# Optimization experiments

Measured on AMD Instinct MI355X. Metric: run time of the kernel, lower is better.

## Reference

```python
import jax, jax.numpy as jnp
import numpy as np

NUM_HEADS = 20


def _rope(t, pos):
    """Rotary embedding (ESM style, rotate_half on full head_dim).
    t: (T, h, d), pos: (T,) float32 position within each sequence."""
    d = t.shape[-1]
    inv_freq = 1.0 / (10000.0 ** (jnp.arange(0, d, 2, dtype=jnp.float32) / d))  # (d/2,)
    freqs = pos[:, None] * inv_freq[None, :]          # (T, d/2)
    emb = jnp.concatenate([freqs, freqs], axis=-1)    # (T, d)
    cos = jnp.cos(emb)[:, None, :]                    # (T, 1, d)
    sin = jnp.sin(emb)[:, None, :]
    x1, x2 = jnp.split(t, 2, axis=-1)
    rot = jnp.concatenate([-x2, x1], axis=-1)
    return t * cos + rot * sin


def setup_inputs() -> dict:
    key = jax.random.key(0)
    ks = jax.random.split(key, 8)
    E = 1280
    lengths = np.array([512, 768, 1024, 1024, 1024, 1280, 1280, 1280], dtype=np.int64)
    cu_lens = jnp.asarray(np.concatenate([[0], np.cumsum(lengths)]).astype(np.int32))
    T = int(lengths.sum())  # 8192
    s = (2.0 / (E + E)) ** 0.5  # xavier-ish scale
    return {
        "x": jax.random.normal(ks[0], (T, E), jnp.float32),
        "cu_lens": cu_lens,
        "max_len": 1280,
        "Wq": jax.random.normal(ks[1], (E, E), jnp.float32) * s,
        "bq": jnp.zeros((E,), jnp.float32),
        "Wk": jax.random.normal(ks[2], (E, E), jnp.float32) * s,
        "bk": jnp.zeros((E,), jnp.float32),
        "Wv": jax.random.normal(ks[3], (E, E), jnp.float32) * s,
        "bv": jnp.zeros((E,), jnp.float32),
        "Wo": jax.random.normal(ks[4], (E, E), jnp.float32) * (2.0 ** 0.5) * s,
        "bo": jnp.zeros((E,), jnp.float32),
    }


def reference(x, cu_lens, max_len, Wq, bq, Wk, bk, Wv, bv, Wo, bo):
    T, E = x.shape
    h = NUM_HEADS
    d = E // h
    scale = d ** -0.5
    # fused QKV projections (q pre-scaled, softmax_scale=1 as in the original)
    q = ((x @ Wq.T + bq) * scale).reshape(T, h, d)
    k = (x @ Wk.T + bk).reshape(T, h, d)
    v = (x @ Wv.T + bv).reshape(T, h, d)
    # per-token sequence id and within-sequence position from cu_lens
    t_idx = jnp.arange(T)
    seq_id = jnp.searchsorted(cu_lens, t_idx, side='right') - 1  # (T,)
    pos = t_idx - cu_lens[seq_id]                                # (T,) int
    # rotary on q and k with per-sequence positions
    posf = pos.astype(jnp.float32)
    q = _rope(q, posf)
    k = _rope(k, posf)
    # scatter packed tokens into padded (B, max_len, h, d) layout
    B = cu_lens.shape[0] - 1
    qp = jnp.zeros((B, max_len, h, d), q.dtype).at[seq_id, pos].set(q)
    kp = jnp.zeros((B, max_len, h, d), k.dtype).at[seq_id, pos].set(k)
    vp = jnp.zeros((B, max_len, h, d), v.dtype).at[seq_id, pos].set(v)
    valid = jnp.zeros((B, max_len), bool).at[seq_id, pos].set(True)
    # non-causal attention within each sequence (block-diagonal over packed tokens)
    scores = jnp.einsum('blhd,bmhd->bhlm', qp, kp)
    scores = jnp.where(valid[:, None, None, :], scores, -1e9)
    attn = jax.nn.softmax(scores, axis=-1)
    o = jnp.einsum('bhlm,bmhd->blhd', attn, vp)
    # gather back to packed layout and apply output projection
    out_tok = o[seq_id, pos].reshape(T, E)
    return out_tok @ Wo.T + bo
```

## Files before the change

kernel.cpp:

```cpp
#include <hip/hip_runtime.h>
#include <hip/hip_bf16.h>
#include <cstdint>

#define E_DIM   1280
#define NHEADS  20
#define HDIM    64
#define QKV_LD  3840

typedef __attribute__((ext_vector_type(8))) short bf8_t;
typedef __attribute__((ext_vector_type(4))) short bf4_t;
typedef __attribute__((ext_vector_type(4))) float f4_t;

__device__ __forceinline__ short f2bs(float f) {
    union { __hip_bfloat16 h; short s; } u;
    u.h = __float2bfloat16(f);
    return u.s;
}

__device__ __forceinline__ bf4_t pk4(f4_t s) {
    union { bf4_t v; uint32_t u[2]; } r;
    asm("v_cvt_pk_bf16_f32 %0, %1, %2" : "=v"(r.u[0]) : "v"(s[0]), "v"(s[1]));
    asm("v_cvt_pk_bf16_f32 %0, %1, %2" : "=v"(r.u[1]) : "v"(s[2]), "v"(s[3]));
    return r.v;
}

__device__ __forceinline__ f4_t mfma16x32(bf8_t a, bf8_t b, f4_t c) {
    return __builtin_amdgcn_mfma_f32_16x16x32_bf16(a, b, c, 0, 0, 0);
}
__device__ __forceinline__ f4_t mfma16x16(bf4_t a, bf4_t b, f4_t c) {
    return __builtin_amdgcn_mfma_f32_16x16x16bf16_1k(a, b, c, 0, 0, 0);
}

__device__ __forceinline__ void gl_lds16(const void* g, void* l) {
    auto gp = reinterpret_cast<__attribute__((address_space(1))) unsigned int*>(
        reinterpret_cast<uintptr_t>(g));
    auto lp = reinterpret_cast<__attribute__((address_space(3))) unsigned int*>(
        reinterpret_cast<uintptr_t>(l));
    __builtin_amdgcn_global_load_lds(gp, lp, 16, 0, 0);
}

#define QSCALE 0.18033688011112042f

__device__ __forceinline__ void cvt8(__hip_bfloat16* dst, const float* src, float sc) {
    float4 a = *(const float4*)src;
    float4 b = *(const float4*)(src + 4);
    bf8_t v;
    v[0] = f2bs(a.x * sc); v[1] = f2bs(a.y * sc); v[2] = f2bs(a.z * sc); v[3] = f2bs(a.w * sc);
    v[4] = f2bs(b.x * sc); v[5] = f2bs(b.y * sc); v[6] = f2bs(b.z * sc); v[7] = f2bs(b.w * sc);
    *(bf8_t*)dst = v;
}

__global__ __launch_bounds__(256) void prep_kernel(
    const float* __restrict__ x,
    const float* __restrict__ wq, const float* __restrict__ wk,
    const float* __restrict__ wv, const float* __restrict__ wo,
    const float* __restrict__ bq, const float* __restrict__ bk, const float* __restrict__ bv,
    __hip_bfloat16* __restrict__ xbf, __hip_bfloat16* __restrict__ wqkv,
    __hip_bfloat16* __restrict__ wobf, float* __restrict__ bqkv,
    long nx8, long nw8, long nb8)
{
    long u = (long)blockIdx.x * 256 + threadIdx.x;
    if (u < nx8) { cvt8(xbf + u * 8, x + u * 8, 1.0f); return; }
    u -= nx8;
    if (u < 3 * nw8) {
        long e = u * 8;
        long w1 = nw8 * 8;
        const float* src; float sc;
        if (e < w1)            { src = wq + e;           sc = QSCALE; }
        else if (e < 2 * w1)   { src = wk + (e - w1);    sc = 1.0f; }
        else                   { src = wv + (e - 2*w1);  sc = 1.0f; }
        cvt8(wqkv + e, src, sc);
        return;
    }
    u -= 3 * nw8;
    if (u < nw8) { cvt8(wobf + u * 8, wo + u * 8, 1.0f); return; }
    u -= nw8;
    if (u < nb8) {
        long e = u * 8;
        #pragma unroll
        for (int j = 0; j < 8; j++) {
            long i = e + j;
            float v;
            if (i < E_DIM)           v = bq[i] * QSCALE;
            else if (i < 2 * E_DIM)  v = bk[i - E_DIM];
            else                     v = bv[i - 2 * E_DIM];
            bqkv[i] = v;
        }
    }
}

template<bool BF16_OUT>
__global__ __launch_bounds__(256, 3) void gemm_nt(
    const __hip_bfloat16* __restrict__ A, const __hip_bfloat16* __restrict__ Bw,
    const float* __restrict__ bias, void* __restrict__ Cout,
    int M, int N, int K, int ldc)
{
    __shared__ __align__(16) __hip_bfloat16 As[128 * 32];
    __shared__ __align__(16) __hip_bfloat16 Bs[128 * 32];
    const int t = threadIdx.x;
    const int wv = t >> 6;
    const int ln = t & 63;
    const int m16 = ln & 15, q4 = ln >> 4;
    const int row0 = blockIdx.y * 128, col0 = blockIdx.x * 128;
    const int wm = (wv >> 1) * 64, wn = (wv & 1) * 64;

    f4_t acc[4][4] = {};

    for (int k0 = 0; k0 < K; k0 += 32) {
        #pragma unroll
        for (int i = 0; i < 2; i++) {
            int s = i * 256 + t;
            int r = s >> 2, c = s & 3;
            gl_lds16(A + (size_t)(row0 + r) * K + k0 + c * 8,
                     As + (size_t)(i * 256 + wv * 64) * 8);
        }
        #pragma unroll
        for (int i = 0; i < 2; i++) {
            int s = i * 256 + t;
            int r = s >> 2, c = s & 3;
            gl_lds16(Bw + (size_t)(col0 + r) * K + k0 + c * 8,
                     Bs + (size_t)(i * 256 + wv * 64) * 8);
        }
        __syncthreads();
        bf8_t af[4], bfr[4];
        #pragma unroll
        for (int mt = 0; mt < 4; mt++)
            af[mt] = *(const bf8_t*)&As[(wm + mt * 16 + m16) * 32 + q4 * 8];
        #pragma unroll
        for (int nt = 0; nt < 4; nt++)
            bfr[nt] = *(const bf8_t*)&Bs[(wn + nt * 16 + m16) * 32 + q4 * 8];
        #pragma unroll
        for (int mt = 0; mt < 4; mt++)
            #pragma unroll
            for (int nt = 0; nt < 4; nt++)
                acc[mt][nt] = mfma16x32(af[mt], bfr[nt], acc[mt][nt]);
        __syncthreads();
    }

    #pragma unroll
    for (int nt = 0; nt < 4; nt++) {
        int cg = col0 + wn + nt * 16 + m16;
        float bv = bias[cg];
        #pragma unroll
        for (int mt = 0; mt < 4; mt++) {
            #pragma unroll
            for (int r = 0; r < 4; r++) {
                int rg = row0 + wm + mt * 16 + q4 * 4 + r;
                float v = acc[mt][nt][r] + bv;
                if constexpr (BF16_OUT)
                    ((__hip_bfloat16*)Cout)[(long)rg * ldc + cg] = __float2bfloat16(v);
                else
                    ((float*)Cout)[(long)rg * ldc + cg] = v;
            }
        }
    }
}

__global__ __launch_bounds__(512, 2) void gemm256(
    const __hip_bfloat16* __restrict__ A, const __hip_bfloat16* __restrict__ Bw,
    const float* __restrict__ bias, __hip_bfloat16* __restrict__ Cout,
    __hip_bfloat16* __restrict__ vtout, int Tdim,
    int M, int N, int K, int ldc)
{
    __shared__ __align__(16) __hip_bfloat16 As[2][256 * 64];
    __shared__ __align__(16) __hip_bfloat16 Bs[2][256 * 64];

    const int t = threadIdx.x;
    const int wv = t >> 6, ln = t & 63;
    const int m16 = ln & 15, q4 = ln >> 4;
    const int wr = wv >> 2, wc = wv & 3;

    const int gx = N >> 8;
    const int nwg = gridDim.x;
    const int id = blockIdx.x;
    const int swz = ((nwg & 7) == 0) ? (id & 7) * (nwg >> 3) + (id >> 3) : id;
    const int col0 = (swz % gx) << 8;
    const int row0 = (swz / gx) << 8;

    const int NT = K >> 6;

    auto stage = [&](const __hip_bfloat16* src, __hip_bfloat16* dst) {
        #pragma unroll
        for (int i = 0; i < 4; i++) {
            int s = i * 512 + t;
            int r = s >> 3, c = (s & 7) ^ (r & 7);
            gl_lds16(src + (size_t)r * K + c * 8,
                     (char*)dst + (size_t)(i * 512 + wv * 64) * 16);
        }
    };

    stage(A  + (size_t)row0 * K,      &As[0][0]);
    stage(Bw + (size_t)col0 * K,      &Bs[0][0]);
    if (NT > 1) {
        stage(A  + (size_t)row0 * K + 64, &As[1][0]);
        stage(Bw + (size_t)col0 * K + 64, &Bs[1][0]);
        asm volatile("s_waitcnt vmcnt(8)" ::: "memory");
    } else {
        asm volatile("s_waitcnt vmcnt(0)" ::: "memory");
    }
    __builtin_amdgcn_s_barrier();

    f4_t acc[8][4] = {};

    for (int kt = 0; kt < NT; kt++) {
        const __hip_bfloat16* Ab = &As[kt & 1][0];
        const __hip_bfloat16* Bb = &Bs[kt & 1][0];

        auto lda = [&](const __hip_bfloat16* base, int r, int kc) {
            return *(const bf8_t*)&base[r * 64 + ((((kc << 2) | q4) ^ (r & 7)) << 3)];
        };

        bf8_t afr[4][2], bf0[2][2], bf1[2][2];
        #pragma unroll
        for (int mt = 0; mt < 4; mt++)
            #pragma unroll
            for (int kc = 0; kc < 2; kc++)
                afr[mt][kc] = lda(Ab, wr * 128 + mt * 16 + m16, kc);
        #pragma unroll
        for (int nt = 0; nt < 2; nt++)
            #pragma unroll
            for (int kc = 0; kc < 2; kc++)
                bf0[nt][kc] = lda(Bb, wc * 64 + nt * 16 + m16, kc);

        __builtin_amdgcn_s_setprio(1);
        #pragma unroll
        for (int mt = 0; mt < 4; mt++)
            #pragma unroll
            for (int nt = 0; nt < 2; nt++)
                #pragma unroll
                for (int kc = 0; kc < 2; kc++)
                    acc[mt][nt] = mfma16x32(afr[mt][kc], bf0[nt][kc], acc[mt][nt]);
        __builtin_amdgcn_s_setprio(0);

        #pragma unroll
        for (int nt = 0; nt < 2; nt++)
            #pragma unroll
            for (int kc = 0; kc < 2; kc++)
                bf1[nt][kc] = lda(Bb, wc * 64 + (2 + nt) * 16 + m16, kc);

        __builtin_amdgcn_s_setprio(1);
        #pragma unroll
        for (int mt = 0; mt < 4; mt++)
            #pragma unroll
            for (int nt = 0; nt < 2; nt++)
                #pragma unroll
                for (int kc = 0; kc < 2; kc++)
                    acc[mt][2 + nt] = mfma16x32(afr[mt][kc], bf1[nt][kc], acc[mt][2 + nt]);
        __builtin_amdgcn_s_setprio(0);

        #pragma unroll
        for (int mt = 0; mt < 4; mt++)
            #pragma unroll
            for (int kc = 0; kc < 2; kc++)
                afr[mt][kc] = lda(Ab, wr * 128 + (4 + mt) * 16 + m16, kc);

        __builtin_amdgcn_s_setprio(1);
        #pragma unroll
        for (int mt = 0; mt < 4; mt++)
            #pragma unroll
            for (int nt = 0; nt < 2; nt++)
                #pragma unroll
                for (int kc = 0; kc < 2; kc++)
                    acc[4 + mt][2 + nt] = mfma16x32(afr[mt][kc], bf1[nt][kc], acc[4 + mt][2 + nt]);
        __builtin_amdgcn_s_setprio(0);

        __builtin_amdgcn_s_setprio(1);
        #pragma unroll
        for (int mt = 0; mt < 4; mt++)
            #pragma unroll
            for (int nt = 0; nt < 2; nt++)
                #pragma unroll
                for (int kc = 0; kc < 2; kc++)
                    acc[4 + mt][nt] = mfma16x32(afr[mt][kc], bf0[nt][kc], acc[4 + mt][nt]);
        __builtin_amdgcn_s_setprio(0);

        asm volatile("s_waitcnt lgkmcnt(0)" ::: "memory");
        __builtin_amdgcn_s_barrier();

        if (kt + 2 < NT) {
            stage(A  + (size_t)row0 * K + (size_t)(kt + 2) * 64, &As[kt & 1][0]);
            stage(Bw + (size_t)col0 * K + (size_t)(kt + 2) * 64, &Bs[kt & 1][0]);
        }
        if (kt + 1 < NT) {
            if (kt + 2 < NT)
                asm volatile("s_waitcnt vmcnt(8)" ::: "memory");
            else
                asm volatile("s_waitcnt vmcnt(0)" ::: "memory");
            __builtin_amdgcn_s_barrier();
        }
    }

    if (col0 >= 2 * E_DIM) {
        #pragma unroll
        for (int nt = 0; nt < 4; nt++) {
            int cg = col0 + wc * 64 + nt * 16 + m16;
            float bval = bias[cg];
            int vrow = cg - 2 * E_DIM;
            #pragma unroll
            for (int mt = 0; mt < 8; mt++) {
                int rg0 = row0 + wr * 128 + mt * 16 + q4 * 4;
                f4_t vv;
                #pragma unroll
                for (int r = 0; r < 4; r++) vv[r] = acc[mt][nt][r] + bval;
                *(bf4_t*)&vtout[(long)vrow * Tdim + rg0] = pk4(vv);
            }
        }
    } else {
        #pragma unroll
        for (int nt = 0; nt < 4; nt++) {
            int cg = col0 + wc * 64 + nt * 16 + m16;
            float bval = bias[cg];
            #pragma unroll
            for (int mt = 0; mt < 8; mt++) {
                #pragma unroll
                for (int r = 0; r < 4; r++) {
                    int rg = row0 + wr * 128 + mt * 16 + q4 * 4 + r;
                    Cout[(long)rg * ldc + cg] = __float2bfloat16(acc[mt][nt][r] + bval);
                }
            }
        }
    }
}

__global__ __launch_bounds__(256) void rope_kernel(
    __hip_bfloat16* __restrict__ qkv, const int* __restrict__ cu, int B, int T)
{
    long idx = (long)blockIdx.x * 256 + threadIdx.x;
    int i = idx & 31;
    long r = idx >> 5;
    int h = (int)(r % NHEADS);
    int tok = (int)(r / NHEADS);
    if (tok >= T) return;
    int pos = tok;
    for (int b = 1; b <= B; b++) if (tok >= cu[b]) pos = tok - cu[b];
    float f = (float)pos * exp2f(-(float)i * 0.41524100558003436f);
    float s, c;
    sincosf(f, &s, &c);
    long base = (long)tok * QKV_LD + h * HDIM + i;
    {
        float q1 = __bfloat162float(qkv[base]);
        float q2 = __bfloat162float(qkv[base + 32]);
        qkv[base]      = __float2bfloat16(q1 * c - q2 * s);
        qkv[base + 32] = __float2bfloat16(q2 * c + q1 * s);
    }
    {
        long kb = base + E_DIM;
        float k1 = __bfloat162float(qkv[kb]);
        float k2 = __bfloat162float(qkv[kb + 32]);
        qkv[kb]      = __float2bfloat16(k1 * c - k2 * s);
        qkv[kb + 32] = __float2bfloat16(k2 * c + k1 * s);
    }
}

__global__ __launch_bounds__(256, 2) void attn_kernel(
    const __hip_bfloat16* __restrict__ qkv, const __hip_bfloat16* __restrict__ vt,
    const int* __restrict__ cu, __hip_bfloat16* __restrict__ obuf, int B, int T)
{
    __shared__ __align__(16) __hip_bfloat16 Ks[2][128 * 64];
    __shared__ __align__(16) __hip_bfloat16 Vs[3][64 * 128];

    int idx = blockIdx.x;
    int h = idx % NHEADS;
    int gt = idx / NHEADS;
    int b = 0, l = 0, seq0 = 0;
    for (; b < B; ++b) {
        seq0 = cu[b];
        l = cu[b + 1] - seq0;
        int ntile = (l + 127) >> 7;
        if (gt < ntile) break;
        gt -= ntile;
    }
    if (b == B) return;
    int q0 = gt * 128;
    const int NT = (l + 127) >> 7;

    const int t = threadIdx.x;
    const int wv = t >> 6, ln = t & 63;
    const int m16 = ln & 15, q4 = ln >> 4;

    auto stage_full = [&](int kv0n, int kb, int vb) {
        #pragma unroll
        for (int i = 0; i < 4; i++) {
            int s2 = i * 256 + t;
            int key = s2 >> 3, cg = (s2 & 7) ^ (key & 7);
            gl_lds16(qkv + (long)(seq0 + kv0n + key) * QKV_LD + E_DIM + h * HDIM + cg * 8,
                     (char*)&Ks[kb][0] + (size_t)(i * 256 + wv * 64) * 16);
        }
        #pragma unroll
        for (int i = 0; i < 4; i++) {
            int s2 = i * 256 + t;
            int d = s2 >> 4, cg = (s2 & 15) ^ (d & 15);
            gl_lds16(vt + (long)(h * HDIM + d) * T + seq0 + kv0n + cg * 8,
                     (char*)&Vs[vb][0] + (size_t)(i * 256 + wv * 64) * 16);
        }
    };
    auto stage_tail = [&](int kv0n, int kb, int vb) {
        #pragma unroll
        for (int i = 0; i < 4; i++) {
            int s2 = i * 256 + t;
            int key = s2 >> 3, c = s2 & 7;
            bf8_t v = (bf8_t)0;
            if (kv0n + key < l)
                v = *(const bf8_t*)(qkv + (long)(seq0 + kv0n + key) * QKV_LD + E_DIM + h * HDIM + c * 8);
            *(bf8_t*)&Ks[kb][key * 64 + (c ^ (key & 7)) * 8] = v;
        }
        #pragma unroll
        for (int i = 0; i < 4; i++) {
            int s2 = i * 256 + t;
            int d = s2 >> 4, c = s2 & 15;
            bf8_t v = (bf8_t)0;
            int tb = kv0n + c * 8;
            #pragma unroll
            for (int u = 0; u < 8; u++)
                if (tb + u < l)
                    v[u] = *(const short*)&vt[(long)(h * HDIM + d) * T + seq0 + tb + u];
            *(bf8_t*)&Vs[vb][d * 128 + (c ^ (d & 15)) * 8] = v;
        }
    };

    if (128 <= l) stage_full(0, 0, 0); else stage_tail(0, 0, 0);

    bf8_t bq[2][2];
    #pragma unroll
    for (int nt = 0; nt < 2; nt++) {
        int qrow = q0 + wv * 32 + nt * 16 + m16;
        #pragma unroll
        for (int kc = 0; kc < 2; kc++) {
            bf8_t v = (bf8_t)0;
            if (qrow < l)
                v = *(const bf8_t*)(qkv + (long)(seq0 + qrow) * QKV_LD + h * HDIM + kc * 32 + q4 * 8);
            bq[nt][kc] = v;
        }
    }

    f4_t oacc[2][4] = {};
    float m_s[2] = {-1e30f, -1e30f};
    float l_s[2] = {0.0f, 0.0f};
    bf4_t bp[8][2];
    int vprev = 0;

    const int ksw0 = (q4 ^ (m16 & 7)) * 8;
    const int ksw1 = ((4 + q4) ^ (m16 & 7)) * 8;

    auto do_pv = [&](const __hip_bfloat16* Vb) {
        __builtin_amdgcn_s_setprio(1);
        #pragma unroll
        for (int mt = 0; mt < 8; mt++) {
            const int vsw = ((mt * 2 + (q4 >> 1)) ^ m16) * 8 + (q4 & 1) * 4;
            #pragma unroll
            for (int dt = 0; dt < 4; dt++) {
                bf4_t av = *(const bf4_t*)&Vb[(dt * 16 + m16) * 128 + vsw];
                #pragma unroll
                for (int nt = 0; nt < 2; nt++)
                    oacc[nt][dt] = mfma16x16(av, bp[mt][nt], oacc[nt][dt]);
            }
        }
        __builtin_amdgcn_s_setprio(0);
    };

    asm volatile("s_waitcnt vmcnt(0) lgkmcnt(0)" ::: "memory");
    __builtin_amdgcn_s_barrier();

    for (int it = 0; it < NT; ++it) {
        const int kv0 = it << 7;
        const bool full = (kv0 + 128 <= l);
        if (it + 1 < NT) {
            int kvn = kv0 + 128;
            if (kvn + 128 <= l) stage_full(kvn, (it + 1) & 1, (it + 1) % 3);
            else stage_tail(kvn, (it + 1) & 1, (it + 1) % 3);
        }
        const __hip_bfloat16* Kb = Ks[it & 1];

        f4_t S[2][8];
        __builtin_amdgcn_s_setprio(1);
        #pragma unroll
        for (int mt = 0; mt < 8; mt++) {
            const __hip_bfloat16* krow = &Kb[(mt * 16 + m16) * 64];
            bf8_t ak0 = *(const bf8_t*)(krow + ksw0);
            bf8_t ak1 = *(const bf8_t*)(krow + ksw1);
            #pragma unroll
            for (int nt = 0; nt < 2; nt++) {
                f4_t a = {};
                a = mfma16x32(ak0, bq[nt][0], a);
                a = mfma16x32(ak1, bq[nt][1], a);
                S[nt][mt] = a;
            }
        }
        __builtin_amdgcn_s_setprio(0);

        if (!full) {
            #pragma unroll
            for (int mt = 0; mt < 8; mt++) {
                #pragma unroll
                for (int r = 0; r < 4; r++) {
                    bool valid = (kv0 + mt * 16 + q4 * 4 + r) < l;
                    #pragma unroll
                    for (int nt = 0; nt < 2; nt++)
                        if (!valid) S[nt][mt][r] = -1e30f;
                }
            }
        }

        if (it > 0) do_pv(Vs[vprev]);

        #pragma unroll
        for (int nt = 0; nt < 2; nt++) {
            float mx = -1e30f;
            #pragma unroll
            for (int mt = 0; mt < 8; mt++)
                #pragma unroll
                for (int r = 0; r < 4; r++)
                    mx = fmaxf(mx, S[nt][mt][r]);
            mx = fmaxf(mx, __shfl_xor(mx, 16));
            mx = fmaxf(mx, __shfl_xor(mx, 32));
            if (!__all(mx - m_s[nt] <= 8.0f)) {
                float mn = fmaxf(m_s[nt], mx);
                float al = exp2f(m_s[nt] - mn);
                m_s[nt] = mn;
                l_s[nt] *= al;
                #pragma unroll
                for (int dt = 0; dt < 4; dt++)
                    #pragma unroll
                    for (int r = 0; r < 4; r++)
                        oacc[nt][dt][r] *= al;
            }
            float mcur = m_s[nt];
            float ls = 0.0f;
            #pragma unroll
            for (int mt = 0; mt < 8; mt++) {
                #pragma unroll
                for (int r = 0; r < 4; r++) {
                    float p = exp2f(S[nt][mt][r] - mcur);
                    ls += p;
                    S[nt][mt][r] = p;
                }
            }
            l_s[nt] += ls;
        }

        #pragma unroll
        for (int mt = 0; mt < 8; mt++)
            #pragma unroll
            for (int nt = 0; nt < 2; nt++)
                bp[mt][nt] = pk4(S[nt][mt]);
        vprev = it % 3;

        if (it + 1 < NT) {
            asm volatile("s_waitcnt vmcnt(0) lgkmcnt(0)" ::: "memory");
            __builtin_amdgcn_s_barrier();
        }
    }

    do_pv(Vs[vprev]);

    #pragma unroll
    for (int nt = 0; nt < 2; nt++) {
        float ls = l_s[nt];
        ls += __shfl_xor(ls, 16);
        ls += __shfl_xor(ls, 32);
        float inv = 1.0f / ls;
        int qrow = q0 + wv * 32 + nt * 16 + m16;
        if (qrow < l) {
            #pragma unroll
            for (int dt = 0; dt < 4; dt++) {
                f4_t o;
                #pragma unroll
                for (int r = 0; r < 4; r++)
                    o[r] = oacc[nt][dt][r] * inv;
                *(bf4_t*)&obuf[(long)(seq0 + qrow) * E_DIM + h * HDIM + dt * 16 + q4 * 4] = pk4(o);
            }
        }
    }
}

extern "C" void kernel_launch(void* const* d_in, const int* in_sizes, int n_in,
                              void* d_out, int out_size, void* d_ws, size_t ws_size,
                              hipStream_t stream) {
    const int E = E_DIM;
    const int T = in_sizes[0] / E;
    const int B = in_sizes[1] - 1;

    const float* x  = (const float*)d_in[0];
    const int*   cu = (const int*)d_in[1];
    const float* Wq = (const float*)d_in[3];
    const float* bq = (const float*)d_in[4];
    const float* Wk = (const float*)d_in[5];
    const float* bk = (const float*)d_in[6];
    const float* Wv = (const float*)d_in[7];
    const float* bv = (const float*)d_in[8];
    const float* Wo = (const float*)d_in[9];
    const float* bo = (const float*)d_in[10];

    char* ws = (char*)d_ws;
    size_t off = 0;
    auto alloc = [&](size_t bytes) -> void* {
        void* p = ws + off;
        off = (off + bytes + 255) & ~(size_t)255;
        return p;
    };
    __hip_bfloat16* xbf   = (__hip_bfloat16*)alloc((size_t)T * E * 2);
    __hip_bfloat16* wqkv  = (__hip_bfloat16*)alloc((size_t)3 * E * E * 2);
    __hip_bfloat16* wobf  = (__hip_bfloat16*)alloc((size_t)E * E * 2);
    float*          bqkv  = (float*)alloc((size_t)3 * E * 4);
    __hip_bfloat16* qkvb  = (__hip_bfloat16*)alloc((size_t)T * 3 * E * 2);
    __hip_bfloat16* vt    = (__hip_bfloat16*)alloc((size_t)E * T * 2);
    __hip_bfloat16* obuf  = xbf;

    long nx8 = (long)T * E / 8;
    long nw8 = (long)E * E / 8;
    long nb8 = (long)3 * E / 8;
    long total = nx8 + 4 * nw8 + nb8;
    int pblocks = (int)((total + 255) / 256);
    prep_kernel<<<pblocks, 256, 0, stream>>>(x, Wq, Wk, Wv, Wo, bq, bk, bv,
                                             xbf, wqkv, wobf, bqkv, nx8, nw8, nb8);

    gemm256<<<(T / 256) * (3 * E / 256), 512, 0, stream>>>(
        xbf, wqkv, bqkv, qkvb, vt, T, T, 3 * E, E, 3 * E);

    rope_kernel<<<(int)(((long)T * NHEADS * 32) / 256), 256, 0, stream>>>(qkvb, cu, B, T);

    int qtiles_ub = T / 128 + B;
    attn_kernel<<<qtiles_ub * NHEADS, 256, 0, stream>>>(qkvb, vt, cu, obuf, B, T);

    gemm_nt<false><<<dim3(E / 128, T / 128), 256, 0, stream>>>(
        obuf, wobf, bo, d_out, T, E, E, E);
}
```

Baseline: 385.9 us.

## Shrink attention KV tile to 64 and drop deferred PV for higher occupancy

Halves the key/value tile from 128 to 64 tokens, cuts LDS from three V buffers to two, and removes the software-pipelined PV step that ran the previous tile's PV MMAs during the current softmax. The launch bound rises from 2 to 4 blocks per SIMD group, with the aim of fitting more waves per CU through lower register and LDS use. In exchange, barriers per key are doubled and the overlap between softmax and PV matrix ops within a wave is lost. The max and sum reductions are also rewritten as trees.

```diff
diff --git a/kernel.cpp b/kernel.cpp
--- a/kernel.cpp
+++ b/kernel.cpp
@@ -352,12 +352,12 @@
     }
 }
 
-__global__ __launch_bounds__(256, 2) void attn_kernel(
+__global__ __launch_bounds__(256, 4) void attn_kernel(
     const __hip_bfloat16* __restrict__ qkv, const __hip_bfloat16* __restrict__ vt,
     const int* __restrict__ cu, __hip_bfloat16* __restrict__ obuf, int B, int T)
 {
-    __shared__ __align__(16) __hip_bfloat16 Ks[2][128 * 64];
-    __shared__ __align__(16) __hip_bfloat16 Vs[3][64 * 128];
+    __shared__ __align__(16) __hip_bfloat16 Ks[2][64 * 64];
+    __shared__ __align__(16) __hip_bfloat16 Vs[2][64 * 64];
 
     int idx = blockIdx.x;
     int h = idx % NHEADS;
@@ -372,53 +372,53 @@
     }
     if (b == B) return;
     int q0 = gt * 128;
-    const int NT = (l + 127) >> 7;
+    const int NT = (l + 63) >> 6;
 
     const int t = threadIdx.x;
     const int wv = t >> 6, ln = t & 63;
     const int m16 = ln & 15, q4 = ln >> 4;
 
-    auto stage_full = [&](int kv0n, int kb, int vb) {
-        #pragma unroll
-        for (int i = 0; i < 4; i++) {
+    auto stage_full = [&](int kv0n, int bi) {
+        #pragma unroll
+        for (int i = 0; i < 2; i++) {
             int s2 = i * 256 + t;
             int key = s2 >> 3, cg = (s2 & 7) ^ (key & 7);
             gl_lds16(qkv + (long)(seq0 + kv0n + key) * QKV_LD + E_DIM + h * HDIM + cg * 8,
-                     (char*)&Ks[kb][0] + (size_t)(i * 256 + wv * 64) * 16);
-        }
-        #pragma unroll
-        for (int i = 0; i < 4; i++) {
+                     (char*)&Ks[bi][0] + (size_t)(i * 256 + wv * 64) * 16);
+        }
+        #pragma unroll
+        for (int i = 0; i < 2; i++) {
             int s2 = i * 256 + t;
-            int d = s2 >> 4, cg = (s2 & 15) ^ (d & 15);
+            int d = s2 >> 3, cg = (s2 & 7) ^ (d & 7);
             gl_lds16(vt + (long)(h * HDIM + d) * T + seq0 + kv0n + cg * 8,
-                     (char*)&Vs[vb][0] + (size_t)(i * 256 + wv * 64) * 16);
+                     (char*)&Vs[bi][0] + (size_t)(i * 256 + wv * 64) * 16);
         }
     };
-    auto stage_tail = [&](int kv0n, int kb, int vb) {
-        #pragma unroll
-        for (int i = 0; i < 4; i++) {
+    auto stage_tail = [&](int kv0n, int bi) {
+        #pragma unroll
+        for (int i = 0; i < 2; i++) {
             int s2 = i * 256 + t;
             int key = s2 >> 3, c = s2 & 7;
             bf8_t v = (bf8_t)0;
             if (kv0n + key < l)
                 v = *(const bf8_t*)(qkv + (long)(seq0 + kv0n + key) * QKV_LD + E_DIM + h * HDIM + c * 8);
-            *(bf8_t*)&Ks[kb][key * 64 + (c ^ (key & 7)) * 8] = v;
-        }
-        #pragma unroll
-        for (int i = 0; i < 4; i++) {
+            *(bf8_t*)&Ks[bi][key * 64 + (c ^ (key & 7)) * 8] = v;
+        }
+        #pragma unroll
+        for (int i = 0; i < 2; i++) {
             int s2 = i * 256 + t;
-            int d = s2 >> 4, c = s2 & 15;
+            int d = s2 >> 3, c = s2 & 7;
             bf8_t v = (bf8_t)0;
             int tb = kv0n + c * 8;
             #pragma unroll
             for (int u = 0; u < 8; u++)
                 if (tb + u < l)
                     v[u] = *(const short*)&vt[(long)(h * HDIM + d) * T + seq0 + tb + u];
-            *(bf8_t*)&Vs[vb][d * 128 + (c ^ (d & 15)) * 8] = v;
+            *(bf8_t*)&Vs[bi][d * 64 + (c ^ (d & 7)) * 8] = v;
         }
     };
 
-    if (128 <= l) stage_full(0, 0, 0); else stage_tail(0, 0, 0);
+    if (64 <= l) stage_full(0, 0); else stage_tail(0, 0);
 
     bf8_t bq[2][2];
     #pragma unroll
@@ -436,45 +436,28 @@
     f4_t oacc[2][4] = {};
     float m_s[2] = {-1e30f, -1e30f};
     float l_s[2] = {0.0f, 0.0f};
-    bf4_t bp[8][2];
-    int vprev = 0;
 
     const int ksw0 = (q4 ^ (m16 & 7)) * 8;
     const int ksw1 = ((4 + q4) ^ (m16 & 7)) * 8;
 
-    auto do_pv = [&](const __hip_bfloat16* Vb) {
-        __builtin_amdgcn_s_setprio(1);
-        #pragma unroll
-        for (int mt = 0; mt < 8; mt++) {
-            const int vsw = ((mt * 2 + (q4 >> 1)) ^ m16) * 8 + (q4 & 1) * 4;
-            #pragma unroll
-            for (int dt = 0; dt < 4; dt++) {
-                bf4_t av = *(const bf4_t*)&Vb[(dt * 16 + m16) * 128 + vsw];
-                #pragma unroll
-                for (int nt = 0; nt < 2; nt++)
-                    oacc[nt][dt] = mfma16x16(av, bp[mt][nt], oacc[nt][dt]);
-            }
-        }
-        __builtin_amdgcn_s_setprio(0);
-    };
-
     asm volatile("s_waitcnt vmcnt(0) lgkmcnt(0)" ::: "memory");
     __builtin_amdgcn_s_barrier();
 
     for (int it = 0; it < NT; ++it) {
-        const int kv0 = it << 7;
-        const bool full = (kv0 + 128 <= l);
+        const int kv0 = it << 6;
+        const bool full = (kv0 + 64 <= l);
         if (it + 1 < NT) {
-            int kvn = kv0 + 128;
-            if (kvn + 128 <= l) stage_full(kvn, (it + 1) & 1, (it + 1) % 3);
-            else stage_tail(kvn, (it + 1) & 1, (it + 1) % 3);
+            int kvn = kv0 + 64;
+            if (kvn + 64 <= l) stage_full(kvn, (it + 1) & 1);
+            else stage_tail(kvn, (it + 1) & 1);
         }
         const __hip_bfloat16* Kb = Ks[it & 1];
-
-        f4_t S[2][8];
+        const __hip_bfloat16* Vb = Vs[it & 1];
+
+        f4_t S[2][4];
         __builtin_amdgcn_s_setprio(1);
         #pragma unroll
-        for (int mt = 0; mt < 8; mt++) {
+        for (int mt = 0; mt < 4; mt++) {
             const __hip_bfloat16* krow = &Kb[(mt * 16 + m16) * 64];
             bf8_t ak0 = *(const bf8_t*)(krow + ksw0);
             bf8_t ak1 = *(const bf8_t*)(krow + ksw1);
@@ -490,7 +473,7 @@
 
         if (!full) {
             #pragma unroll
-            for (int mt = 0; mt < 8; mt++) {
+            for (int mt = 0; mt < 4; mt++) {
                 #pragma unroll
                 for (int r = 0; r < 4; r++) {
                     bool valid = (kv0 + mt * 16 + q4 * 4 + r) < l;
@@ -501,16 +484,14 @@
             }
         }
 
-        if (it > 0) do_pv(Vs[vprev]);
-
         #pragma unroll
         for (int nt = 0; nt < 2; nt++) {
-            float mx = -1e30f;
-            #pragma unroll
-            for (int mt = 0; mt < 8; mt++)
-                #pragma unroll
-                for (int r = 0; r < 4; r++)
-                    mx = fmaxf(mx, S[nt][mt][r]);
+            float pm[4];
+            #pragma unroll
+            for (int mt = 0; mt < 4; mt++)
+                pm[mt] = fmaxf(fmaxf(S[nt][mt][0], S[nt][mt][1]),
+                               fmaxf(S[nt][mt][2], S[nt][mt][3]));
+            float mx = fmaxf(fmaxf(pm[0], pm[1]), fmaxf(pm[2], pm[3]));
             mx = fmaxf(mx, __shfl_xor(mx, 16));
             mx = fmaxf(mx, __shfl_xor(mx, 32));
             if (!__all(mx - m_s[nt] <= 8.0f)) {
@@ -525,33 +506,40 @@
                         oacc[nt][dt][r] *= al;
             }
             float mcur = m_s[nt];
-            float ls = 0.0f;
-            #pragma unroll
-            for (int mt = 0; mt < 8; mt++) {
-                #pragma unroll
-                for (int r = 0; r < 4; r++) {
-                    float p = exp2f(S[nt][mt][r] - mcur);
-                    ls += p;
-                    S[nt][mt][r] = p;
-                }
-            }
-            l_s[nt] += ls;
-        }
-
-        #pragma unroll
-        for (int mt = 0; mt < 8; mt++)
-            #pragma unroll
-            for (int nt = 0; nt < 2; nt++)
-                bp[mt][nt] = pk4(S[nt][mt]);
-        vprev = it % 3;
+            float ps[4];
+            #pragma unroll
+            for (int mt = 0; mt < 4; mt++) {
+                f4_t p;
+                p[0] = exp2f(S[nt][mt][0] - mcur);
+                p[1] = exp2f(S[nt][mt][1] - mcur);
+                p[2] = exp2f(S[nt][mt][2] - mcur);
+                p[3] = exp2f(S[nt][mt][3] - mcur);
+                S[nt][mt] = p;
+                ps[mt] = (p[0] + p[1]) + (p[2] + p[3]);
+            }
+            l_s[nt] += (ps[0] + ps[1]) + (ps[2] + ps[3]);
+        }
+
+        __builtin_amdgcn_s_setprio(1);
+        #pragma unroll
+        for (int mt = 0; mt < 4; mt++) {
+            bf4_t bp0 = pk4(S[0][mt]);
+            bf4_t bp1 = pk4(S[1][mt]);
+            const int vsw = ((mt * 2 + (q4 >> 1)) ^ (m16 & 7)) * 8 + (q4 & 1) * 4;
+            #pragma unroll
+            for (int dt = 0; dt < 4; dt++) {
+                bf4_t av = *(const bf4_t*)&Vb[(dt * 16 + m16) * 64 + vsw];
+                oacc[0][dt] = mfma16x16(av, bp0, oacc[0][dt]);
+                oacc[1][dt] = mfma16x16(av, bp1, oacc[1][dt]);
+            }
+        }
+        __builtin_amdgcn_s_setprio(0);
 
         if (it + 1 < NT) {
             asm volatile("s_waitcnt vmcnt(0) lgkmcnt(0)" ::: "memory");
             __builtin_amdgcn_s_barrier();
         }
     }
-
-    do_pv(Vs[vprev]);
 
     #pragma unroll
     for (int nt = 0; nt < 2; nt++) {
```

Measured after the change: 384.4 us. About the same (-0.4%).
